# Kernel optimization log

Hardware: AMD Instinct MI355X
Metric: run time of the kernel (lower is better)

Reference implementation:

```python
import jax, jax.numpy as jnp
import numpy as np
from jax import lax

B, N, C = 16, 16384, 256
NP, NS = 128, 16        # num_proposal, nsample
R = 0.3                 # ball radius (normalize_xyz divides by R)


def setup_inputs() -> dict:
    key = jax.random.key(0)
    ks = jax.random.split(key, 11)
    f32 = jnp.float32
    return dict(
        vote_xyz=jax.random.uniform(ks[0], (B, N, 3), f32),
        vote_features=jax.random.normal(ks[1], (B, C, N), f32),
        # SA shared-MLP 1x1 conv weights (bias folded into BN), mlp=[259,128,128,128]
        W1=jax.random.normal(ks[2], (128, C + 3), f32) * 0.05,
        W2=jax.random.normal(ks[3], (128, 128), f32) * 0.05,
        W3=jax.random.normal(ks[4], (128, 128), f32) * 0.05,
        sa_bn_scale=jax.random.uniform(ks[5], (3, 128), f32, 0.5, 1.5),
        sa_bn_bias=jax.random.normal(ks[6], (3, 128), f32) * 0.1,
        # trailing mlp_module: two Conv1d(128,128,1)+BN(eval)+ReLU
        Wm=jax.random.normal(ks[7], (2, 128, 128), f32) * 0.05,
        bm=jax.random.normal(ks[8], (2, 128), f32) * 0.01,
        m_bn_scale=jax.random.uniform(ks[9], (2, 128), f32, 0.5, 1.5),
        m_bn_bias=jax.random.normal(ks[10], (2, 128), f32) * 0.1,
    )


def _fps(xyz):
    # farthest point sampling, one cloud: xyz [N,3] -> inds [NP]
    def body(carry, _):
        mind, last = carry
        d = jnp.sum((xyz - xyz[last]) ** 2, axis=-1)
        mind = jnp.minimum(mind, d)
        nxt = jnp.argmax(mind).astype(jnp.int32)
        return (mind, nxt), nxt
    init = (jnp.full((xyz.shape[0],), 1e10, xyz.dtype), jnp.int32(0))
    _, rest = lax.scan(body, init, None, length=NP - 1)
    return jnp.concatenate([jnp.zeros((1,), jnp.int32), rest])


def _ball_query(xyz, centers):
    # xyz [N,3], centers [NP,3] -> idx [NP,NS]; first NS in-ball points in
    # original order, padded with the first in-ball index (pointnet2 semantics)
    d2 = jnp.sum((centers[:, None, :] - xyz[None, :, :]) ** 2, axis=-1)  # [NP,N]
    n = xyz.shape[0]
    cand = jnp.where(d2 < R * R, jnp.arange(n, dtype=jnp.int32), jnp.int32(n))
    firstk = jnp.sort(cand, axis=-1)[:, :NS]                             # [NP,NS]
    first = firstk[:, :1]
    idx = jnp.where(firstk == n, first, firstk)
    return jnp.where(idx == n, 0, idx)


def _forward(vote_xyz, vote_features, W1, W2, W3, sa_bn_scale, sa_bn_bias,
             Wm, bm, m_bn_scale, m_bn_bias):
    fps_inds = jax.vmap(_fps)(vote_xyz)                                   # [B,NP]
    new_xyz = jnp.take_along_axis(vote_xyz, fps_inds[..., None], axis=1)  # [B,NP,3]
    idx = jax.vmap(_ball_query)(vote_xyz, new_xyz)                        # [B,NP,NS]
    grouped_xyz = jax.vmap(lambda p, i: p[i])(vote_xyz, idx)              # [B,NP,NS,3]
    grouped_xyz = (grouped_xyz - new_xyz[:, :, None, :]) / R              # normalize_xyz
    grouped_feat = jax.vmap(lambda f, i: f[:, i])(vote_features, idx)     # [B,C,NP,NS]
    g = jnp.concatenate([grouped_xyz.transpose(0, 3, 1, 2), grouped_feat], axis=1)  # [B,C+3,NP,NS]
    for W, s, b in ((W1, sa_bn_scale[0], sa_bn_bias[0]),
                    (W2, sa_bn_scale[1], sa_bn_bias[1]),
                    (W3, sa_bn_scale[2], sa_bn_bias[2])):
        g = jax.nn.relu(jnp.einsum('bcsn,oc->bosn', g, W)
                        * s[None, :, None, None] + b[None, :, None, None])
    feat = jnp.max(g, axis=-1)                                            # [B,128,NP] max pool
    for k in range(2):
        feat = jax.nn.relu((jnp.einsum('bcs,oc->bos', feat, Wm[k]) + bm[k][None, :, None])
                           * m_bn_scale[k][None, :, None] + m_bn_bias[k][None, :, None])
    return new_xyz, feat, fps_inds


def reference(vote_xyz, vote_features, W1, W2, W3, sa_bn_scale, sa_bn_bias,
              Wm, bm, m_bn_scale, m_bn_bias):
    return _forward(vote_xyz, vote_features, W1, W2, W3, sa_bn_scale, sa_bn_bias,
                    Wm, bm, m_bn_scale, m_bn_bias)
```

## Files before the change

kernel.cpp:

```cpp
#include <hip/hip_runtime.h>
#include <hip/hip_bf16.h>

#define NB  16
#define NN  16384
#define NC  256
#define NPP 128
#define NSS 16

#define FTH 1024
#define FPT 16

__global__ __launch_bounds__(256) void transpose_kernel(
    const float* __restrict__ W1, const float* __restrict__ W2,
    const float* __restrict__ W3, const float* __restrict__ Wm,
    float* __restrict__ W1T, float* __restrict__ W2T,
    float* __restrict__ W3T, float* __restrict__ WmT) {
  int i = blockIdx.x * 256 + threadIdx.x;
  if (i < 128 * 259) { int o = i / 259, c = i - o * 259; W1T[c * 128 + o] = W1[i]; }
  if (i < 128 * 128) {
    int o = i >> 7, c = i & 127;
    W2T[c * 128 + o] = W2[i];
    W3T[c * 128 + o] = W3[i];
    WmT[c * 128 + o] = Wm[i];
    WmT[16384 + c * 128 + o] = Wm[16384 + i];
  }
}

__global__ __attribute__((amdgpu_flat_work_group_size(1024, 1024),
                          amdgpu_waves_per_eu(4, 4)))
void fps_kernel(
    const float* __restrict__ xyz,
    float* __restrict__ centers, float* __restrict__ out_xyz,
    float* __restrict__ out_indf) {
  int b = blockIdx.x;
  const float* px = xyz + (size_t)b * (NN * 3);
  int t = threadIdx.x;
  float X[FPT], Y[FPT], Z[FPT], MD[FPT];
#pragma unroll
  for (int j = 0; j < FPT; ++j) {
    int n = t + j * FTH;
    float x = px[n * 3 + 0];
    float y = px[n * 3 + 1];
    float z = px[n * 3 + 2];
    asm volatile("" : "+v"(x), "+v"(y), "+v"(z));
    X[j] = x; Y[j] = y; Z[j] = z;
    MD[j] = 1e10f;
  }
  __shared__ unsigned long long cand[2][16];
  float cx = px[0], cy = px[1], cz = px[2];
  if (t == 0) {
    out_indf[b * NPP] = 0.0f;
    centers[(b * NPP) * 3 + 0] = cx;
    centers[(b * NPP) * 3 + 1] = cy;
    centers[(b * NPP) * 3 + 2] = cz;
    out_xyz[(b * NPP) * 3 + 0] = cx;
    out_xyz[(b * NPP) * 3 + 1] = cy;
    out_xyz[(b * NPP) * 3 + 2] = cz;
  }
  for (int it = 1; it < NPP; ++it) {
    float bv = -1.0f;
    int bi = 0;
#pragma unroll
    for (int j = 0; j < FPT; ++j) {
      float dx = __fsub_rn(X[j], cx);
      float dy = __fsub_rn(Y[j], cy);
      float dz = __fsub_rn(Z[j], cz);
      float d  = __fadd_rn(__fadd_rn(__fmul_rn(dx, dx), __fmul_rn(dy, dy)),
                           __fmul_rn(dz, dz));
      float m = fminf(MD[j], d);
      MD[j] = m;
      if (m > bv) { bv = m; bi = t + j * FTH; }
    }
    unsigned long long pk =
        (((unsigned long long)__float_as_uint(bv)) << 32) |
        (unsigned long long)(0xFFFFFFFFu - (unsigned)bi);
#define STEP_ROR(N)                                                         \
    {                                                                       \
      unsigned lo = (unsigned)pk, hi = (unsigned)(pk >> 32);                \
      lo = (unsigned)__builtin_amdgcn_mov_dpp((int)lo, 0x120 | N, 0xF, 0xF, true); \
      hi = (unsigned)__builtin_amdgcn_mov_dpp((int)hi, 0x120 | N, 0xF, 0xF, true); \
      unsigned long long o = ((unsigned long long)hi << 32) | lo;           \
      if (o > pk) pk = o;                                                   \
    }
    STEP_ROR(1) STEP_ROR(2) STEP_ROR(4) STEP_ROR(8)
#undef STEP_ROR
    {
      unsigned lo = (unsigned)pk, hi = (unsigned)(pk >> 32);
      lo = (unsigned)__builtin_amdgcn_ds_swizzle((int)lo, 0x401F);
      hi = (unsigned)__builtin_amdgcn_ds_swizzle((int)hi, 0x401F);
      unsigned long long o = ((unsigned long long)hi << 32) | lo;
      if (o > pk) pk = o;
    }
    {
      unsigned long long o = __shfl_xor(pk, 32, 64);
      if (o > pk) pk = o;
    }
    if ((t & 63) == 0) cand[it & 1][t >> 6] = pk;
    __syncthreads();
    const unsigned long long* cp = cand[it & 1];
    unsigned long long mx = cp[0];
#pragma unroll
    for (int w = 1; w < 16; ++w) {
      unsigned long long v = cp[w];
      if (v > mx) mx = v;
    }
    int win = (int)(0xFFFFFFFFu - (unsigned)(mx & 0xFFFFFFFFull));
    win = __builtin_amdgcn_readfirstlane(win);
    cx = px[win * 3 + 0];
    cy = px[win * 3 + 1];
    cz = px[win * 3 + 2];
    if (t == 0) {
      out_indf[b * NPP + it] = (float)win;
      centers[(b * NPP + it) * 3 + 0] = cx;
      centers[(b * NPP + it) * 3 + 1] = cy;
      centers[(b * NPP + it) * 3 + 2] = cz;
      out_xyz[(b * NPP + it) * 3 + 0] = cx;
      out_xyz[(b * NPP + it) * 3 + 1] = cy;
      out_xyz[(b * NPP + it) * 3 + 2] = cz;
    }
  }
}

__global__ __launch_bounds__(64) void ballq_kernel(
    const float* __restrict__ xyz, const float* __restrict__ centers,
    int* __restrict__ bidx) {
  int bs = blockIdx.x;
  int b = bs >> 7;
  int lane = threadIdx.x;
  const float* px = xyz + (size_t)b * (NN * 3);
  float cx = centers[bs * 3 + 0];
  float cy = centers[bs * 3 + 1];
  float cz = centers[bs * 3 + 2];
  __shared__ int coll[NSS];
  const float rr = 0.09f;
  int have = 0;
  for (int c0 = 0; c0 < NN; c0 += 64) {
    int n = c0 + lane;
    float dx = __fsub_rn(px[n * 3 + 0], cx);
    float dy = __fsub_rn(px[n * 3 + 1], cy);
    float dz = __fsub_rn(px[n * 3 + 2], cz);
    float d2 = __fadd_rn(__fadd_rn(__fmul_rn(dx, dx), __fmul_rn(dy, dy)),
                         __fmul_rn(dz, dz));
    bool in = d2 < rr;
    unsigned long long m = __ballot(in);
    if (in) {
      int pos = have + __popcll(m & ((1ull << lane) - 1ull));
      if (pos < NSS) coll[pos] = n;
    }
    have += __popcll(m);
    if (have >= NSS) break;
  }
  __syncthreads();
  int first = coll[0];
  if (lane < NSS) bidx[bs * NSS + lane] = (lane < have) ? coll[lane] : first;
}

__device__ __forceinline__ void layer_f(const float (*in)[20], int cin,
                                        const float* __restrict__ WT,
                                        const float* __restrict__ sc,
                                        const float* __restrict__ bi,
                                        int o2, int k0, float4& r0, float4& r1) {
  float a0[4] = {0.f, 0.f, 0.f, 0.f};
  float a1[4] = {0.f, 0.f, 0.f, 0.f};
  for (int c = 0; c < cin; ++c) {
    float2 w = *(const float2*)(WT + c * 128 + o2);
    float4 gv = *(const float4*)(&in[c][k0]);
    a0[0] = fmaf(w.x, gv.x, a0[0]);
    a0[1] = fmaf(w.x, gv.y, a0[1]);
    a0[2] = fmaf(w.x, gv.z, a0[2]);
    a0[3] = fmaf(w.x, gv.w, a0[3]);
    a1[0] = fmaf(w.y, gv.x, a1[0]);
    a1[1] = fmaf(w.y, gv.y, a1[1]);
    a1[2] = fmaf(w.y, gv.z, a1[2]);
    a1[3] = fmaf(w.y, gv.w, a1[3]);
  }
  float s0 = sc[o2], s1 = sc[o2 + 1], b0 = bi[o2], b1 = bi[o2 + 1];
  r0.x = fmaxf(fmaf(a0[0], s0, b0), 0.f);
  r0.y = fmaxf(fmaf(a0[1], s0, b0), 0.f);
  r0.z = fmaxf(fmaf(a0[2], s0, b0), 0.f);
  r0.w = fmaxf(fmaf(a0[3], s0, b0), 0.f);
  r1.x = fmaxf(fmaf(a1[0], s1, b1), 0.f);
  r1.y = fmaxf(fmaf(a1[1], s1, b1), 0.f);
  r1.z = fmaxf(fmaf(a1[2], s1, b1), 0.f);
  r1.w = fmaxf(fmaf(a1[3], s1, b1), 0.f);
}

__global__ __launch_bounds__(256) void mlp_kernel(
    const float* __restrict__ xyz, const float* __restrict__ feats,
    const float* __restrict__ centers, const int* __restrict__ bidx,
    const float* __restrict__ W1T, const float* __restrict__ W2T,
    const float* __restrict__ W3T, const float* __restrict__ sa_sc,
    const float* __restrict__ sa_bi, float* __restrict__ feat0) {
  int bs = blockIdx.x;
  int b = bs >> 7;
  int s = bs & 127;
  int tid = threadIdx.x;
  __shared__ float g[259][20];
  __shared__ float h1[128][20];
  __shared__ float h2[128][20];
  __shared__ int kidx[NSS];
  __shared__ float ctr[3];
  if (tid < NSS) kidx[tid] = bidx[bs * NSS + tid];
  if (tid < 3) ctr[tid] = centers[bs * 3 + tid];
  __syncthreads();
  const float* px = xyz + (size_t)b * (NN * 3);
  if (tid < NSS) {
    int n = kidx[tid];
    g[0][tid] = __fdiv_rn(__fsub_rn(px[n * 3 + 0], ctr[0]), 0.3f);
    g[1][tid] = __fdiv_rn(__fsub_rn(px[n * 3 + 1], ctr[1]), 0.3f);
    g[2][tid] = __fdiv_rn(__fsub_rn(px[n * 3 + 2], ctr[2]), 0.3f);
  }
  {
    const float* row = feats + ((size_t)b * NC + tid) * NN;
#pragma unroll
    for (int k = 0; k < NSS; ++k) g[3 + tid][k] = row[kidx[k]];
  }
  __syncthreads();
  int o2 = (tid & 63) * 2;
  int k0 = (tid >> 6) * 4;
  float4 r0, r1;
  layer_f(g, 259, W1T, sa_sc, sa_bi, o2, k0, r0, r1);
  *(float4*)&h1[o2][k0] = r0;
  *(float4*)&h1[o2 + 1][k0] = r1;
  __syncthreads();
  layer_f(h1, 128, W2T, sa_sc + 128, sa_bi + 128, o2, k0, r0, r1);
  *(float4*)&h2[o2][k0] = r0;
  *(float4*)&h2[o2 + 1][k0] = r1;
  __syncthreads();
  layer_f(h2, 128, W3T, sa_sc + 256, sa_bi + 256, o2, k0, r0, r1);
  float m0 = fmaxf(fmaxf(r0.x, r0.y), fmaxf(r0.z, r0.w));
  float m1 = fmaxf(fmaxf(r1.x, r1.y), fmaxf(r1.z, r1.w));
  int w = tid >> 6;
  h1[o2][w] = m0;
  h1[o2 + 1][w] = m1;
  __syncthreads();
  if (tid < 128) {
    float m = fmaxf(fmaxf(h1[tid][0], h1[tid][1]), fmaxf(h1[tid][2], h1[tid][3]));
    feat0[((size_t)b * 128 + tid) * 128 + s] = m;
  }
}

__global__ __launch_bounds__(256) void head_kernel(
    const float* __restrict__ feat0, const float* __restrict__ WmT,
    const float* __restrict__ bm, const float* __restrict__ msc,
    const float* __restrict__ mbi, float* __restrict__ out_feat) {
  int blk = blockIdx.x;
  int b = blk >> 2;
  int sbase = (blk & 3) * 32;
  int tid = threadIdx.x;
  __shared__ float fa[128][36];
  __shared__ float fb[128][36];
  {
    int sj = tid & 31, c0 = tid >> 5;
    for (int c = c0; c < 128; c += 8)
      fa[c][sj] = feat0[((size_t)b * 128 + c) * 128 + sbase + sj];
  }
  __syncthreads();
  int o2 = (tid & 63) * 2, s0 = (tid >> 6) * 8;
  float a0[8], a1[8];
#pragma unroll
  for (int j = 0; j < 8; ++j) { a0[j] = 0.f; a1[j] = 0.f; }
  for (int c = 0; c < 128; ++c) {
    float2 w = *(const float2*)&WmT[c * 128 + o2];
    float4 f0 = *(const float4*)&fa[c][s0];
    float4 f1 = *(const float4*)&fa[c][s0 + 4];
    a0[0] = fmaf(w.x, f0.x, a0[0]); a0[1] = fmaf(w.x, f0.y, a0[1]);
    a0[2] = fmaf(w.x, f0.z, a0[2]); a0[3] = fmaf(w.x, f0.w, a0[3]);
    a0[4] = fmaf(w.x, f1.x, a0[4]); a0[5] = fmaf(w.x, f1.y, a0[5]);
    a0[6] = fmaf(w.x, f1.z, a0[6]); a0[7] = fmaf(w.x, f1.w, a0[7]);
    a1[0] = fmaf(w.y, f0.x, a1[0]); a1[1] = fmaf(w.y, f0.y, a1[1]);
    a1[2] = fmaf(w.y, f0.z, a1[2]); a1[3] = fmaf(w.y, f0.w, a1[3]);
    a1[4] = fmaf(w.y, f1.x, a1[4]); a1[5] = fmaf(w.y, f1.y, a1[5]);
    a1[6] = fmaf(w.y, f1.z, a1[6]); a1[7] = fmaf(w.y, f1.w, a1[7]);
  }
  {
    float c0 = bm[o2], c1 = bm[o2 + 1];
    float t0 = msc[o2], t1 = msc[o2 + 1];
    float q0 = mbi[o2], q1 = mbi[o2 + 1];
#pragma unroll
    for (int j = 0; j < 8; ++j) {
      fb[o2][s0 + j]     = fmaxf(fmaf(a0[j] + c0, t0, q0), 0.f);
      fb[o2 + 1][s0 + j] = fmaxf(fmaf(a1[j] + c1, t1, q1), 0.f);
    }
  }
  __syncthreads();
#pragma unroll
  for (int j = 0; j < 8; ++j) { a0[j] = 0.f; a1[j] = 0.f; }
  for (int c = 0; c < 128; ++c) {
    float2 w = *(const float2*)&WmT[16384 + c * 128 + o2];
    float4 f0 = *(const float4*)&fb[c][s0];
    float4 f1 = *(const float4*)&fb[c][s0 + 4];
    a0[0] = fmaf(w.x, f0.x, a0[0]); a0[1] = fmaf(w.x, f0.y, a0[1]);
    a0[2] = fmaf(w.x, f0.z, a0[2]); a0[3] = fmaf(w.x, f0.w, a0[3]);
    a0[4] = fmaf(w.x, f1.x, a0[4]); a0[5] = fmaf(w.x, f1.y, a0[5]);
    a0[6] = fmaf(w.x, f1.z, a0[6]); a0[7] = fmaf(w.x, f1.w, a0[7]);
    a1[0] = fmaf(w.y, f0.x, a1[0]); a1[1] = fmaf(w.y, f0.y, a1[1]);
    a1[2] = fmaf(w.y, f0.z, a1[2]); a1[3] = fmaf(w.y, f0.w, a1[3]);
    a1[4] = fmaf(w.y, f1.x, a1[4]); a1[5] = fmaf(w.y, f1.y, a1[5]);
    a1[6] = fmaf(w.y, f1.z, a1[6]); a1[7] = fmaf(w.y, f1.w, a1[7]);
  }
  {
    float c0 = bm[128 + o2], c1 = bm[128 + o2 + 1];
    float t0 = msc[128 + o2], t1 = msc[128 + o2 + 1];
    float q0 = mbi[128 + o2], q1 = mbi[128 + o2 + 1];
    float4 v0a, v0b, v1a, v1b;
    v0a.x = fmaxf(fmaf(a0[0] + c0, t0, q0), 0.f);
    v0a.y = fmaxf(fmaf(a0[1] + c0, t0, q0), 0.f);
    v0a.z = fmaxf(fmaf(a0[2] + c0, t0, q0), 0.f);
    v0a.w = fmaxf(fmaf(a0[3] + c0, t0, q0), 0.f);
    v0b.x = fmaxf(fmaf(a0[4] + c0, t0, q0), 0.f);
    v0b.y = fmaxf(fmaf(a0[5] + c0, t0, q0), 0.f);
    v0b.z = fmaxf(fmaf(a0[6] + c0, t0, q0), 0.f);
    v0b.w = fmaxf(fmaf(a0[7] + c0, t0, q0), 0.f);
    v1a.x = fmaxf(fmaf(a1[0] + c1, t1, q1), 0.f);
    v1a.y = fmaxf(fmaf(a1[1] + c1, t1, q1), 0.f);
    v1a.z = fmaxf(fmaf(a1[2] + c1, t1, q1), 0.f);
    v1a.w = fmaxf(fmaf(a1[3] + c1, t1, q1), 0.f);
    v1b.x = fmaxf(fmaf(a1[4] + c1, t1, q1), 0.f);
    v1b.y = fmaxf(fmaf(a1[5] + c1, t1, q1), 0.f);
    v1b.z = fmaxf(fmaf(a1[6] + c1, t1, q1), 0.f);
    v1b.w = fmaxf(fmaf(a1[7] + c1, t1, q1), 0.f);
    float* p0 = &out_feat[((size_t)b * 128 + o2) * 128 + sbase + s0];
    float* p1 = &out_feat[((size_t)b * 128 + o2 + 1) * 128 + sbase + s0];
    *(float4*)p0 = v0a;
    *(float4*)(p0 + 4) = v0b;
    *(float4*)p1 = v1a;
    *(float4*)(p1 + 4) = v1b;
  }
}

extern "C" void kernel_launch(void* const* d_in, const int* in_sizes, int n_in,
                              void* d_out, int out_size, void* d_ws, size_t ws_size,
                              hipStream_t stream) {
  const float* vote_xyz  = (const float*)d_in[0];
  const float* vote_feat = (const float*)d_in[1];
  const float* W1   = (const float*)d_in[2];
  const float* W2   = (const float*)d_in[3];
  const float* W3   = (const float*)d_in[4];
  const float* sasc = (const float*)d_in[5];
  const float* sabi = (const float*)d_in[6];
  const float* Wm   = (const float*)d_in[7];
  const float* bm   = (const float*)d_in[8];
  const float* msc  = (const float*)d_in[9];
  const float* mbi  = (const float*)d_in[10];

  float* out = (float*)d_out;
  float* out_xyz  = out;
  float* out_feat = out + 6144;
  float* out_indf = out + 6144 + 262144;

  char* ws = (char*)d_ws;
  float* centers = (float*)(ws + 8192);
  int*   bidx    = (int*)(ws + 32768);
  float* W1T     = (float*)(ws + 163840);
  float* W2T     = (float*)(ws + 296448);
  float* W3T     = (float*)(ws + 361984);
  float* WmT     = (float*)(ws + 427520);
  float* feat0   = (float*)(ws + 558592);

  hipLaunchKernelGGL(transpose_kernel, dim3(130), dim3(256), 0, stream,
                     W1, W2, W3, Wm, W1T, W2T, W3T, WmT);
  hipLaunchKernelGGL(fps_kernel, dim3(NB), dim3(FTH), 0, stream,
                     vote_xyz, centers, out_xyz, out_indf);
  hipLaunchKernelGGL(ballq_kernel, dim3(NB * NPP), dim3(64), 0, stream,
                     vote_xyz, centers, bidx);
  hipLaunchKernelGGL(mlp_kernel, dim3(NB * NPP), dim3(256), 0, stream,
                     vote_xyz, vote_feat, centers, bidx, W1T, W2T, W3T,
                     sasc, sabi, feat0);
  hipLaunchKernelGGL(head_kernel, dim3(NB * 4), dim3(256), 0, stream,
                     feat0, WmT, bm, msc, mbi, out_feat);
}
```

Baseline: 410.4 us.

## Move FPS x/y coordinates to LDS and reduce wave candidates with DPP

The FPS kernel now keeps x and y coordinates in a 128KB shared-memory float2 array and holds only z and min-distance in registers. This cuts VGPR pressure, and the winner's x/y is read from LDS instead of global memory. The per-iteration scan over the 16 wave candidates is replaced by a 16-lane DPP row reduction, and the argmax tracks the slot index j rather than the full point index. The trade is one LDS read per point per iteration, which may cost more than the reduced register and latency overhead saves.

```diff
diff --git a/kernel.cpp b/kernel.cpp
--- a/kernel.cpp
+++ b/kernel.cpp
@@ -35,18 +35,20 @@
   int b = blockIdx.x;
   const float* px = xyz + (size_t)b * (NN * 3);
   int t = threadIdx.x;
-  float X[FPT], Y[FPT], Z[FPT], MD[FPT];
+  __shared__ float2 sxy[NN];
+  __shared__ unsigned long long cand[2][16];
+  float Zr[FPT], MD[FPT];
 #pragma unroll
   for (int j = 0; j < FPT; ++j) {
     int n = t + j * FTH;
     float x = px[n * 3 + 0];
     float y = px[n * 3 + 1];
     float z = px[n * 3 + 2];
-    asm volatile("" : "+v"(x), "+v"(y), "+v"(z));
-    X[j] = x; Y[j] = y; Z[j] = z;
+    asm volatile("" : "+v"(z));
+    sxy[n] = make_float2(x, y);
+    Zr[j] = z;
     MD[j] = 1e10f;
   }
-  __shared__ unsigned long long cand[2][16];
   float cx = px[0], cy = px[1], cz = px[2];
   if (t == 0) {
     out_indf[b * NPP] = 0.0f;
@@ -57,23 +59,26 @@
     out_xyz[(b * NPP) * 3 + 1] = cy;
     out_xyz[(b * NPP) * 3 + 2] = cz;
   }
+  __syncthreads();
   for (int it = 1; it < NPP; ++it) {
     float bv = -1.0f;
-    int bi = 0;
+    int bj = 0;
 #pragma unroll
     for (int j = 0; j < FPT; ++j) {
-      float dx = __fsub_rn(X[j], cx);
-      float dy = __fsub_rn(Y[j], cy);
-      float dz = __fsub_rn(Z[j], cz);
+      float2 v = sxy[t + j * FTH];
+      float dx = __fsub_rn(v.x, cx);
+      float dy = __fsub_rn(v.y, cy);
+      float dz = __fsub_rn(Zr[j], cz);
       float d  = __fadd_rn(__fadd_rn(__fmul_rn(dx, dx), __fmul_rn(dy, dy)),
                            __fmul_rn(dz, dz));
       float m = fminf(MD[j], d);
       MD[j] = m;
-      if (m > bv) { bv = m; bi = t + j * FTH; }
-    }
+      if (m > bv) { bv = m; bj = j; }
+    }
+    int bi = t + bj * FTH;
     unsigned long long pk =
         (((unsigned long long)__float_as_uint(bv)) << 32) |
-        (unsigned long long)(0xFFFFFFFFu - (unsigned)bi);
+        (unsigned long long)(~(unsigned)bi);
 #define STEP_ROR(N)                                                         \
     {                                                                       \
       unsigned lo = (unsigned)pk, hi = (unsigned)(pk >> 32);                \
@@ -83,7 +88,6 @@
       if (o > pk) pk = o;                                                   \
     }
     STEP_ROR(1) STEP_ROR(2) STEP_ROR(4) STEP_ROR(8)
-#undef STEP_ROR
     {
       unsigned lo = (unsigned)pk, hi = (unsigned)(pk >> 32);
       lo = (unsigned)__builtin_amdgcn_ds_swizzle((int)lo, 0x401F);
@@ -97,17 +101,14 @@
     }
     if ((t & 63) == 0) cand[it & 1][t >> 6] = pk;
     __syncthreads();
-    const unsigned long long* cp = cand[it & 1];
-    unsigned long long mx = cp[0];
-#pragma unroll
-    for (int w = 1; w < 16; ++w) {
-      unsigned long long v = cp[w];
-      if (v > mx) mx = v;
-    }
-    int win = (int)(0xFFFFFFFFu - (unsigned)(mx & 0xFFFFFFFFull));
+    pk = cand[it & 1][t & 15];
+    STEP_ROR(1) STEP_ROR(2) STEP_ROR(4) STEP_ROR(8)
+#undef STEP_ROR
+    int win = (int)(~(unsigned)(pk & 0xFFFFFFFFull));
     win = __builtin_amdgcn_readfirstlane(win);
-    cx = px[win * 3 + 0];
-    cy = px[win * 3 + 1];
+    float2 wv = sxy[win];
+    cx = wv.x;
+    cy = wv.y;
     cz = px[win * 3 + 2];
     if (t == 0) {
       out_indf[b * NPP + it] = (float)win;
```

Measured after the change: 404.0 us. About the same (-1.6%).
